# Optimization experiments

Measured on AMD Instinct MI355X. Metric: run time of the kernel, lower is better.

## Reference

```python
import jax, jax.numpy as jnp
import numpy as np

B = 4096
NC = 64        # n_concepts
NT = 16        # n_tasks
H = 256        # prior_units (prior_layers = 1)
HID = 256      # prior_hids = [256, 256]
K = 20         # n_components
IN = 3 * NC + NT + 1        # GRU input size = 209
MLP_IN = H + 3 * NC + NT    # rnn_out input = 464
LOG_2PI = float(np.log(2.0 * np.pi))


def setup_inputs() -> dict:
    key = jax.random.key(0)
    ks = jax.random.split(key, 16)
    s = 0.05
    inp = {
        "z": jax.random.normal(ks[0], (B, NC), jnp.float32),
        "c": jax.random.normal(ks[1], (B, NC + NT), jnp.float32),
        "b": (jax.random.uniform(ks[2], (B, NC)) < 0.5).astype(jnp.float32),
        "m": (jax.random.uniform(ks[3], (B, NC)) < 0.5).astype(jnp.float32),
        # GRU (PyTorch layout: gates ordered r, z, n)
        "W_ih": jax.random.normal(ks[4], (3 * H, IN), jnp.float32) * s,
        "W_hh": jax.random.normal(ks[5], (3 * H, H), jnp.float32) * s,
        "b_ih": jax.random.normal(ks[6], (3 * H,), jnp.float32) * s,
        "b_hh": jax.random.normal(ks[7], (3 * H,), jnp.float32) * s,
        # rnn_out MLP: Linear(464,256)+Tanh, Linear(256,256)+Tanh, Linear(256,3K)
        "W1": jax.random.normal(ks[8], (HID, MLP_IN), jnp.float32) * s,
        "b1": jax.random.normal(ks[9], (HID,), jnp.float32) * s,
        "W2": jax.random.normal(ks[10], (HID, HID), jnp.float32) * s,
        "b2": jax.random.normal(ks[11], (HID,), jnp.float32) * s,
        "W3": jax.random.normal(ks[12], (3 * K, HID), jnp.float32) * s,
        "b3": jax.random.normal(ks[13], (3 * K,), jnp.float32) * s,
    }
    return inp


def _logp(z, c, b, m, W_ih, W_hh, b_ih, b_hh, W1, b1, W2, b2, W3, b3):
    Bsz, d = z.shape
    cbm = jnp.concatenate([c, b, m], axis=1)               # [B, 3*NC+NT]
    # z input at step t is -1 for t=0, else z[:, t-1]
    z_prev = jnp.concatenate(
        [-jnp.ones((Bsz, 1), z.dtype), z[:, :-1]], axis=1)  # [B, d]
    # Precompute the input-gate projections for all steps without
    # materializing the full [d, B, IN] sequence tensor:
    # column 0 of W_ih multiplies z_prev; the rest multiplies cbm.
    gi_cbm = cbm @ W_ih[:, 1:].T + b_ih                    # [B, 3H]
    gi = gi_cbm[None, :, :] + z_prev.T[:, :, None] * W_ih[:, 0][None, None, :]  # [d, B, 3H]

    def gru_step(h, gi_t):
        gh = h @ W_hh.T + b_hh
        gi_r, gi_u, gi_n = jnp.split(gi_t, 3, axis=-1)
        gh_r, gh_u, gh_n = jnp.split(gh, 3, axis=-1)
        r = jax.nn.sigmoid(gi_r + gh_r)
        u = jax.nn.sigmoid(gi_u + gh_u)
        n = jnp.tanh(gi_n + r * gh_n)
        h_new = (1.0 - u) * n + u * h
        return h_new, h_new

    h0 = jnp.zeros((Bsz, W_hh.shape[1]), z.dtype)
    _, hs = jax.lax.scan(gru_step, h0, gi)                 # [d, B, H]
    hs = jnp.transpose(hs, (1, 0, 2))                      # [B, d, H]

    feat = jnp.concatenate(
        [hs, jnp.broadcast_to(cbm[:, None, :], (Bsz, d, cbm.shape[1]))],
        axis=2)                                            # [B, d, MLP_IN]
    h1 = jnp.tanh(feat @ W1.T + b1)
    h2 = jnp.tanh(h1 @ W2.T + b2)
    params = h2 @ W3.T + b3                                # [B, d, 3K]

    logits, means, lsigmas = jnp.split(params, 3, axis=-1)
    t = z[..., None]                                       # [B, d, 1]
    log_norm = -lsigmas - 0.5 * LOG_2PI
    diff = (t - means) * jnp.exp(-lsigmas)
    log_kernel = -0.5 * jnp.square(diff)
    log_like = (jax.nn.logsumexp(log_kernel + log_norm + logits, axis=-1)
                - jax.nn.logsumexp(logits, axis=-1))       # [B, d]

    query = m * (1.0 - b)
    mask = jnp.sort(query, axis=1)[:, ::-1]                # descending sort of values
    return jnp.sum(log_like * mask, axis=1)                # [B]


def reference(z, c, b, m, W_ih, W_hh, b_ih, b_hh, W1, b1, W2, b2, W3, b3):
    return _logp(z, c, b, m, W_ih, W_hh, b_ih, b_hh,
                 W1, b1, W2, b2, W3, b3)
```

## Files before the change

kernel.cpp:

```cpp
#include <hip/hip_runtime.h>
#include <hip/hip_bf16.h>

#define BATCH  4096
#define NCC    64
#define HDIM   256
#define G3     768
#define NROW   (BATCH*NCC)
#define NK     20
#define LOG2PI 1.8378770664093453f

typedef __attribute__((ext_vector_type(8))) short bf16x8;
typedef __attribute__((ext_vector_type(4))) float f32x4;

__device__ __forceinline__ float sigm(float x) { return 1.0f/(1.0f + __expf(-x)); }
__device__ __forceinline__ float tanh_fast(float x) { return 1.0f - 2.0f/(__expf(2.0f*x) + 1.0f); }
__device__ __forceinline__ unsigned short f2bf(float x) {
  __hip_bfloat16 h = __float2bfloat16(x);
  return __builtin_bit_cast(unsigned short, h);
}
__device__ __forceinline__ int swz(int r) { return (r & 7) ^ ((r & 8) >> 2); }

__global__ __launch_bounds__(256) void k_cvtall(
    const float* __restrict__ c, const float* __restrict__ bv,
    const float* __restrict__ mv, const float* __restrict__ W_ih,
    const float* __restrict__ W_hh, const float* __restrict__ W1,
    const float* __restrict__ W2, const float* __restrict__ W3,
    unsigned short* __restrict__ cbmB, unsigned short* __restrict__ CW,
    unsigned short* __restrict__ WhhB, unsigned short* __restrict__ W1aB,
    unsigned short* __restrict__ W2B, unsigned short* __restrict__ W3pB,
    float* __restrict__ w0) {
  int idx = blockIdx.x*256 + threadIdx.x;
  if (idx < 1048576) {
    int row = idx >> 8, k = idx & 255;
    float v = 0.f;
    if (k < 80)       v = c [row*80 + k];
    else if (k < 144) v = bv[row*64 + (k-80)];
    else if (k < 208) v = mv[row*64 + (k-144)];
    cbmB[idx] = f2bf(v);
    return;
  }
  idx -= 1048576;
  if (idx < 262144) {
    int n = idx >> 8, k = idx & 255;
    float v = 0.f;
    if (n < 768) { if (k < 208) v = W_ih[n*209 + 1 + k]; }
    else         { if (k < 208) v = W1[(n-768)*464 + 256 + k]; }
    CW[idx] = f2bf(v);
    return;
  }
  idx -= 262144;
  if (idx < 196608) { WhhB[idx] = f2bf(W_hh[idx]); return; }
  idx -= 196608;
  if (idx < 65536) { int n = idx>>8, k = idx&255; W1aB[idx] = f2bf(W1[n*464+k]); return; }
  idx -= 65536;
  if (idx < 65536) { W2B[idx] = f2bf(W2[idx]); return; }
  idx -= 65536;
  if (idx < 16384) {
    int n = idx >> 8;
    float v = 0.f;
    if (n < 60) v = W3[idx];
    W3pB[idx] = f2bf(v);
    return;
  }
  idx -= 16384;
  if (idx < 768) w0[idx] = W_ih[idx*209];
}

__global__ __launch_bounds__(512) void k_pre(
    const unsigned short* __restrict__ A, const unsigned short* __restrict__ Bw,
    const float* __restrict__ b_ih, const float* __restrict__ b_hh,
    const float* __restrict__ b1,
    float* __restrict__ gi, float* __restrict__ P1) {
  __shared__ __align__(16) unsigned short As[128*64];
  __shared__ __align__(16) unsigned short Bs[128*64];
  int tid = threadIdx.x;
  int rb = blockIdx.x >> 3, cb = blockIdx.x & 7;
  long row0 = (long)rb * 128;
  int n0 = cb * 128;
  int wv = tid >> 6, lane = tid & 63;
  int lq = lane >> 4, l16 = lane & 15;
  int wrg = wv & 3, wcg = wv >> 2;
  f32x4 acc[2][4];
#pragma unroll
  for (int i = 0; i < 2; ++i)
#pragma unroll
    for (int j = 0; j < 4; ++j) acc[i][j] = (f32x4){0.f,0.f,0.f,0.f};
  for (int kb = 0; kb < 256; kb += 64) {
#pragma unroll
    for (int i = 0; i < 2; ++i) {
      int s = i*512 + tid;
      int r = s >> 3, cg = (s & 7) ^ (r & 7);
      *(uint4*)&As[s*8] = *(const uint4*)&A[(row0 + r)*256 + kb + cg*8];
      *(uint4*)&Bs[s*8] = *(const uint4*)&Bw[(long)(n0 + r)*256 + kb + cg*8];
    }
    __syncthreads();
#pragma unroll
    for (int kc = 0; kc < 2; ++kc) {
      int csel = kc*4 + lq;
      bf16x8 af[2];
#pragma unroll
      for (int rt = 0; rt < 2; ++rt) {
        int r = wrg*32 + rt*16 + l16;
        af[rt] = *(const bf16x8*)&As[r*64 + ((csel ^ (r & 7)))*8];
      }
#pragma unroll
      for (int ct = 0; ct < 4; ++ct) {
        int n = wcg*64 + ct*16 + l16;
        bf16x8 bfr = *(const bf16x8*)&Bs[n*64 + ((csel ^ (n & 7)))*8];
        acc[0][ct] = __builtin_amdgcn_mfma_f32_16x16x32_bf16(af[0], bfr, acc[0][ct], 0, 0, 0);
        acc[1][ct] = __builtin_amdgcn_mfma_f32_16x16x32_bf16(af[1], bfr, acc[1][ct], 0, 0, 0);
      }
    }
    __syncthreads();
  }
#pragma unroll
  for (int rt = 0; rt < 2; ++rt)
#pragma unroll
    for (int q = 0; q < 4; ++q) {
      long row = row0 + wrg*32 + rt*16 + lq*4 + q;
#pragma unroll
      for (int ct = 0; ct < 4; ++ct) {
        int n = n0 + wcg*64 + ct*16 + l16;
        float v = acc[rt][ct][q];
        if (n < 512)      gi[row*G3 + n] = v + b_ih[n] + b_hh[n];
        else if (n < 768) gi[row*G3 + n] = v + b_ih[n];
        else              P1[row*256 + (n-768)] = v + b1[n-768];
      }
    }
}

__global__ __attribute__((amdgpu_flat_work_group_size(512, 512)))
__attribute__((amdgpu_waves_per_eu(2, 2)))
void k_gru(
    const float* __restrict__ z, const float* __restrict__ gi,
    const unsigned short* __restrict__ WhhB, const float* __restrict__ b_hh,
    const float* __restrict__ w0, unsigned short* __restrict__ hs) {
  __shared__ __align__(16) unsigned short hbf[2*16*256];
  __shared__ __align__(16) float gis[768*20];
  __shared__ __align__(16) float zs[64*16];
  __shared__ float wls[768 + 256];
  int tid = threadIdx.x;
  int wv = tid >> 6, lane = tid & 63;
  int lq = lane >> 4, l16 = lane & 15;
  int row0 = blockIdx.x * 16;
  bf16x8 wf[6][8];
#pragma unroll
  for (int g = 0; g < 3; ++g)
#pragma unroll
    for (int tt = 0; tt < 2; ++tt)
#pragma unroll
      for (int ks = 0; ks < 8; ++ks)
        wf[g*2+tt][ks] = *(const bf16x8*)&WhhB[(long)(g*256 + wv*32 + tt*16 + l16)*256 + ks*32 + lq*8];
  for (int i = tid; i < 768; i += 512) wls[i] = w0[i];
  for (int i = tid; i < 256; i += 512) wls[768 + i] = b_hh[512 + i];
  for (int i = tid; i < 1024; i += 512) {
    int t = i >> 4, r = i & 15;
    zs[i] = z[(row0+r)*64 + t];
  }
#pragma unroll
  for (int i = 0; i < 24; ++i) {
    int s = i*512 + tid;
    int r = s / 768, cc = s - r*768;
    gis[cc*20 + r] = gi[(long)(row0+r)*768 + cc];
  }
  for (int i = tid; i < 2048; i += 512) ((unsigned int*)hbf)[i] = 0u;
  float hp[2][4] = {{0.f,0.f,0.f,0.f},{0.f,0.f,0.f,0.f}};
  const int s7 = l16 & 7;
  const int arow = l16*256;
  const int r4 = lq*4;
  const int hc0 = wv*32 + l16;
  const int cr = tid >> 5, ccc = tid & 31;
  const int csrc = cr*256 + ((ccc ^ (cr & 7)))*8;
  unsigned short* cbase = hs + (long)(row0+cr)*64*256 + ccc*8;
  __syncthreads();
#pragma unroll 1
  for (int t = 0; t < 64; ++t) {
    const int co = (t & 1) << 12;
    const int no = co ^ 4096;
    float zp[4];
    {
      float4 zv4 = *(const float4*)&zs[(t ? (t-1) : 0)*16 + r4];
#pragma unroll
      for (int q = 0; q < 4; ++q) zp[q] = t ? (&zv4.x)[q] : -1.0f;
    }
    f32x4 a[6];
#pragma unroll
    for (int tt = 0; tt < 2; ++tt) {
      int hc = hc0 + tt*16;
      f32x4 gR = *(const f32x4*)&gis[hc*20 + r4];
      f32x4 gU = *(const f32x4*)&gis[(256+hc)*20 + r4];
      float w0r = wls[hc], w0u = wls[256+hc], bn = wls[768 + hc];
#pragma unroll
      for (int q = 0; q < 4; ++q) {
        a[tt][q]   = gR[q] + zp[q]*w0r;
        a[2+tt][q] = gU[q] + zp[q]*w0u;
        a[4+tt][q] = bn;
      }
    }
#pragma unroll
    for (int ks = 0; ks < 8; ++ks) {
      bf16x8 af = *(const bf16x8*)&hbf[co + arow + (((ks*4+lq) ^ s7))*8];
#pragma unroll
      for (int f = 0; f < 6; ++f)
        a[f] = __builtin_amdgcn_mfma_f32_16x16x32_bf16(af, wf[f][ks], a[f], 0, 0, 0);
    }
    if (t) {
      uint4 cdat = *(const uint4*)&hbf[co + csrc];
      *(uint4*)(cbase + (t-1)*256) = cdat;
    }
#pragma unroll
    for (int tt = 0; tt < 2; ++tt) {
      int hc = hc0 + tt*16;
      int hchunk = hc >> 3, hlow = hc & 7;
      float w0n = wls[512 + hc];
      f32x4 gN = *(const f32x4*)&gis[(512+hc)*20 + r4];
#pragma unroll
      for (int q = 0; q < 4; ++q) {
        int r = r4 + q;
        float rr = sigm(a[tt][q]);
        float uu = sigm(a[2+tt][q]);
        float nn = tanh_fast(gN[q] + zp[q]*w0n + rr*a[4+tt][q]);
        float hn = uu*(hp[tt][q] - nn) + nn;
        hp[tt][q] = hn;
        hbf[no + r*256 + ((hchunk ^ (r & 7)))*8 + hlow] = f2bf(hn);
      }
    }
    __syncthreads();
  }
  uint4 cdat = *(const uint4*)&hbf[0 + csrc];
  *(uint4*)(cbase + 63*256) = cdat;
}

__global__ __launch_bounds__(512) void k_l1(
    const unsigned short* __restrict__ A, const unsigned short* __restrict__ Bw,
    const float* __restrict__ P1, unsigned short* __restrict__ Out) {
  __shared__ __align__(16) unsigned short As[128*64];
  __shared__ __align__(16) unsigned short Bs[256*64];
  int tid = threadIdx.x;
  long row0 = (long)blockIdx.x * 128;
  int wv = tid >> 6, lane = tid & 63;
  int lq = lane >> 4, l16 = lane & 15;
  int wrg = wv & 3, wcg = wv >> 2;
  f32x4 acc[2][8];
#pragma unroll
  for (int i = 0; i < 2; ++i)
#pragma unroll
    for (int j = 0; j < 8; ++j) acc[i][j] = (f32x4){0.f,0.f,0.f,0.f};
  for (int kb = 0; kb < 256; kb += 64) {
#pragma unroll
    for (int i = 0; i < 2; ++i) {
      int s = i*512 + tid;
      int r = s >> 3, cg = (s & 7) ^ (r & 7);
      *(uint4*)&As[s*8] = *(const uint4*)&A[(row0 + r)*256 + kb + cg*8];
    }
#pragma unroll
    for (int i = 0; i < 4; ++i) {
      int s = i*512 + tid;
      int r = s >> 3, cg = (s & 7) ^ (r & 7);
      *(uint4*)&Bs[s*8] = *(const uint4*)&Bw[(long)r*256 + kb + cg*8];
    }
    __syncthreads();
#pragma unroll
    for (int kc = 0; kc < 2; ++kc) {
      int csel = kc*4 + lq;
      bf16x8 af[2];
#pragma unroll
      for (int rt = 0; rt < 2; ++rt) {
        int r = wrg*32 + rt*16 + l16;
        af[rt] = *(const bf16x8*)&As[r*64 + ((csel ^ (r & 7)))*8];
      }
#pragma unroll
      for (int ct = 0; ct < 8; ++ct) {
        int n = wcg*128 + ct*16 + l16;
        bf16x8 bfr = *(const bf16x8*)&Bs[n*64 + ((csel ^ (n & 7)))*8];
        acc[0][ct] = __builtin_amdgcn_mfma_f32_16x16x32_bf16(af[0], bfr, acc[0][ct], 0, 0, 0);
        acc[1][ct] = __builtin_amdgcn_mfma_f32_16x16x32_bf16(af[1], bfr, acc[1][ct], 0, 0, 0);
      }
    }
    __syncthreads();
  }
#pragma unroll
  for (int rt = 0; rt < 2; ++rt)
#pragma unroll
    for (int q = 0; q < 4; ++q) {
      long row = row0 + wrg*32 + rt*16 + lq*4 + q;
#pragma unroll
      for (int ct = 0; ct < 8; ++ct) {
        int n = wcg*128 + ct*16 + l16;
        float b = P1[(row >> 6)*256 + n];
        Out[row*256 + n] = f2bf(tanh_fast(acc[rt][ct][q] + b));
      }
    }
}

__global__ __launch_bounds__(512) void k_l23(
    const unsigned short* __restrict__ A, const unsigned short* __restrict__ W2B,
    const float* __restrict__ b2, const unsigned short* __restrict__ W3pB,
    const float* __restrict__ b3, const float* __restrict__ z,
    float* __restrict__ ll) {
  __shared__ __align__(16) unsigned short As[128*64];
  __shared__ __align__(16) unsigned short Bs[256*64];
  __shared__ __align__(16) unsigned short h2s[128*256];
  int tid = threadIdx.x;
  long row0 = (long)blockIdx.x * 128;
  int wv = tid >> 6, lane = tid & 63;
  int lq = lane >> 4, l16 = lane & 15;
  int wrg = wv & 3, wcg = wv >> 2;
  f32x4 acc[2][8];
#pragma unroll
  for (int i = 0; i < 2; ++i)
#pragma unroll
    for (int j = 0; j < 8; ++j) acc[i][j] = (f32x4){0.f,0.f,0.f,0.f};
  for (int kb = 0; kb < 256; kb += 64) {
#pragma unroll
    for (int i = 0; i < 2; ++i) {
      int s = i*512 + tid;
      int r = s >> 3, cg = (s & 7) ^ (r & 7);
      *(uint4*)&As[s*8] = *(const uint4*)&A[(row0 + r)*256 + kb + cg*8];
    }
#pragma unroll
    for (int i = 0; i < 4; ++i) {
      int s = i*512 + tid;
      int r = s >> 3, cg = (s & 7) ^ (r & 7);
      *(uint4*)&Bs[s*8] = *(const uint4*)&W2B[(long)r*256 + kb + cg*8];
    }
    __syncthreads();
#pragma unroll
    for (int kc = 0; kc < 2; ++kc) {
      int csel = kc*4 + lq;
      bf16x8 af[2];
#pragma unroll
      for (int rt = 0; rt < 2; ++rt) {
        int r = wrg*32 + rt*16 + l16;
        af[rt] = *(const bf16x8*)&As[r*64 + ((csel ^ (r & 7)))*8];
      }
#pragma unroll
      for (int ct = 0; ct < 8; ++ct) {
        int n = wcg*128 + ct*16 + l16;
        bf16x8 bfr = *(const bf16x8*)&Bs[n*64 + ((csel ^ (n & 7)))*8];
        acc[0][ct] = __builtin_amdgcn_mfma_f32_16x16x32_bf16(af[0], bfr, acc[0][ct], 0, 0, 0);
        acc[1][ct] = __builtin_amdgcn_mfma_f32_16x16x32_bf16(af[1], bfr, acc[1][ct], 0, 0, 0);
      }
    }
    __syncthreads();
  }
#pragma unroll
  for (int rt = 0; rt < 2; ++rt)
#pragma unroll
    for (int q = 0; q < 4; ++q) {
      int lr = wrg*32 + rt*16 + lq*4 + q;
#pragma unroll
      for (int ct = 0; ct < 8; ++ct) {
        int n = wcg*128 + ct*16 + l16;
        h2s[lr*256 + (((n >> 3) ^ swz(lr))*8 + (n & 7))] =
            f2bf(tanh_fast(acc[rt][ct][q] + b2[n]));
      }
    }
#pragma unroll
  for (int i = 0; i < 4; ++i) {
    int s = i*512 + tid;
    int r = s >> 5, cc = s & 31;
    *(uint4*)&Bs[r*256 + ((cc ^ swz(r)))*8] = *(const uint4*)&W3pB[r*256 + cc*8];
  }
  __syncthreads();
  f32x4 pacc[4];
#pragma unroll
  for (int j = 0; j < 4; ++j) pacc[j] = (f32x4){0.f,0.f,0.f,0.f};
#pragma unroll
  for (int ks = 0; ks < 8; ++ks) {
    int chunk = ks*4 + lq;
    int ar = wv*16 + l16;
    bf16x8 af = *(const bf16x8*)&h2s[ar*256 + ((chunk ^ swz(ar)))*8];
#pragma unroll
    for (int ct = 0; ct < 4; ++ct) {
      int br = ct*16 + l16;
      bf16x8 bfr = *(const bf16x8*)&Bs[br*256 + ((chunk ^ swz(br)))*8];
      pacc[ct] = __builtin_amdgcn_mfma_f32_16x16x32_bf16(af, bfr, pacc[ct], 0, 0, 0);
    }
  }
  float* Ps = (float*)&h2s[wv*16*256];
#pragma unroll
  for (int ct = 0; ct < 4; ++ct) {
    int n = ct*16 + l16;
    float b = (n < 60) ? b3[n] : 0.0f;
#pragma unroll
    for (int q = 0; q < 4; ++q)
      Ps[(lq*4 + q)*68 + n] = pacc[ct][q] + b;
  }
  if (lane < 16) {
    long grow = row0 + wv*16 + lane;
    float zv = z[grow];
    const float* p = &Ps[lane*68];
    float mx1 = -1e30f;
#pragma unroll
    for (int i = 0; i < NK; ++i) mx1 = fmaxf(mx1, p[i]);
    float s1 = 0.0f;
#pragma unroll
    for (int i = 0; i < NK; ++i) s1 += __expf(p[i] - mx1);
    float lse1 = mx1 + __logf(s1);
    float a[NK];
    float mx2 = -1e30f;
#pragma unroll
    for (int i = 0; i < NK; ++i) {
      float lg = p[i], me = p[20+i], ls = p[40+i];
      float e = __expf(-ls);
      float d = (zv - me) * e;
      float ai = -0.5f*d*d - ls - 0.5f*LOG2PI + lg;
      a[i] = ai;
      mx2 = fmaxf(mx2, ai);
    }
    float s2 = 0.0f;
#pragma unroll
    for (int i = 0; i < NK; ++i) s2 += __expf(a[i] - mx2);
    float lse2 = mx2 + __logf(s2);
    ll[grow] = lse2 - lse1;
  }
}

__global__ __launch_bounds__(256) void k_final(const float* __restrict__ bv,
    const float* __restrict__ mv, const float* __restrict__ ll,
    float* __restrict__ out) {
  int tid = threadIdx.x;
  int wave = tid >> 6, lane = tid & 63;
  int b = blockIdx.x*4 + wave;
  float q = mv[b*64 + lane] * (1.0f - bv[b*64 + lane]);
  unsigned long long bal = __ballot(q > 0.5f);
  int S = __popcll(bal);
  float val = (lane < S) ? ll[(long)b*64 + lane] : 0.0f;
#pragma unroll
  for (int off = 32; off > 0; off >>= 1) val += __shfl_down(val, off);
  if (lane == 0) out[b] = val;
}

extern "C" void kernel_launch(void* const* d_in, const int* in_sizes, int n_in,
                              void* d_out, int out_size, void* d_ws, size_t ws_size,
                              hipStream_t stream) {
  const float* z    = (const float*)d_in[0];
  const float* c    = (const float*)d_in[1];
  const float* bv   = (const float*)d_in[2];
  const float* mv   = (const float*)d_in[3];
  const float* W_ih = (const float*)d_in[4];
  const float* W_hh = (const float*)d_in[5];
  const float* b_ih = (const float*)d_in[6];
  const float* b_hh = (const float*)d_in[7];
  const float* W1   = (const float*)d_in[8];
  const float* b1   = (const float*)d_in[9];
  const float* W2   = (const float*)d_in[10];
  const float* b2   = (const float*)d_in[11];
  const float* W3   = (const float*)d_in[12];
  const float* b3   = (const float*)d_in[13];
  float* out = (float*)d_out;

  char* p = (char*)d_ws;
  auto alloc = [&](size_t bytes) {
    char* q = p;
    p += (bytes + 255) & ~(size_t)255;
    return q;
  };
  unsigned short* cbmB = (unsigned short*)alloc((size_t)BATCH*256*2);
  unsigned short* CW   = (unsigned short*)alloc((size_t)1024*256*2);
  unsigned short* WhhB = (unsigned short*)alloc((size_t)G3*256*2);
  unsigned short* W1aB = (unsigned short*)alloc((size_t)256*256*2);
  unsigned short* W2B  = (unsigned short*)alloc((size_t)256*256*2);
  unsigned short* W3pB = (unsigned short*)alloc((size_t)64*256*2);
  float* w0 = (float*)alloc((size_t)G3*4);
  float* gi = (float*)alloc((size_t)BATCH*G3*4);
  float* P1 = (float*)alloc((size_t)BATCH*256*4);
  float* ll = (float*)alloc((size_t)NROW*4);
  unsigned short* hs = (unsigned short*)alloc((size_t)NROW*HDIM*2);

  k_cvtall<<<6468, 256, 0, stream>>>(c, bv, mv, W_ih, W_hh, W1, W2, W3,
                                     cbmB, CW, WhhB, W1aB, W2B, W3pB, w0);
  k_pre<<<256, 512, 0, stream>>>(cbmB, CW, b_ih, b_hh, b1, gi, P1);
  k_gru<<<256, 512, 0, stream>>>(z, gi, WhhB, b_hh, w0, hs);
  k_l1<<<NROW/128, 512, 0, stream>>>(hs, W1aB, P1, hs);
  k_l23<<<NROW/128, 512, 0, stream>>>(hs, W2B, b2, W3pB, b3, z, ll);
  k_final<<<BATCH/4, 256, 0, stream>>>(bv, mv, ll, out);
}
```

Baseline: 517.2 us.

## Halve GRU block to 256 threads with each wave holding twice the weight columns

```diff
diff --git a/kernel.cpp b/kernel.cpp
--- a/kernel.cpp
+++ b/kernel.cpp
@@ -129,8 +129,8 @@
     }
 }
 
-__global__ __attribute__((amdgpu_flat_work_group_size(512, 512)))
-__attribute__((amdgpu_waves_per_eu(2, 2)))
+__global__ __attribute__((amdgpu_flat_work_group_size(256, 256)))
+__attribute__((amdgpu_waves_per_eu(1, 1)))
 void k_gru(
     const float* __restrict__ z, const float* __restrict__ gi,
     const unsigned short* __restrict__ WhhB, const float* __restrict__ b_hh,
@@ -143,36 +143,59 @@
   int wv = tid >> 6, lane = tid & 63;
   int lq = lane >> 4, l16 = lane & 15;
   int row0 = blockIdx.x * 16;
-  bf16x8 wf[6][8];
+
+  bf16x8 wf[3][4][8];
 #pragma unroll
   for (int g = 0; g < 3; ++g)
 #pragma unroll
-    for (int tt = 0; tt < 2; ++tt)
+    for (int cf = 0; cf < 4; ++cf)
 #pragma unroll
       for (int ks = 0; ks < 8; ++ks)
-        wf[g*2+tt][ks] = *(const bf16x8*)&WhhB[(long)(g*256 + wv*32 + tt*16 + l16)*256 + ks*32 + lq*8];
-  for (int i = tid; i < 768; i += 512) wls[i] = w0[i];
-  for (int i = tid; i < 256; i += 512) wls[768 + i] = b_hh[512 + i];
-  for (int i = tid; i < 1024; i += 512) {
+        wf[g][cf][ks] = *(const bf16x8*)&WhhB[
+            (long)(g*256 + wv*64 + cf*16 + l16)*256 + ks*32 + lq*8];
+
+  for (int i = tid; i < 768; i += 256) wls[i] = w0[i];
+  for (int i = tid; i < 256; i += 256) wls[768 + i] = b_hh[512 + i];
+  for (int i = tid; i < 1024; i += 256) {
     int t = i >> 4, r = i & 15;
     zs[i] = z[(row0+r)*64 + t];
   }
 #pragma unroll
-  for (int i = 0; i < 24; ++i) {
-    int s = i*512 + tid;
-    int r = s / 768, cc = s - r*768;
-    gis[cc*20 + r] = gi[(long)(row0+r)*768 + cc];
-  }
-  for (int i = tid; i < 2048; i += 512) ((unsigned int*)hbf)[i] = 0u;
-  float hp[2][4] = {{0.f,0.f,0.f,0.f},{0.f,0.f,0.f,0.f}};
+  for (int i = 0; i < 12; ++i) {
+    int s = i*256 + tid;
+    int r = s / 192, c4 = (s - r*192)*4;
+    float4 v = *(const float4*)&gi[(long)(row0+r)*768 + c4];
+    gis[(c4+0)*20 + r] = v.x;
+    gis[(c4+1)*20 + r] = v.y;
+    gis[(c4+2)*20 + r] = v.z;
+    gis[(c4+3)*20 + r] = v.w;
+  }
+  for (int i = tid; i < 2048; i += 256) ((unsigned int*)hbf)[i] = 0u;
+
+#pragma unroll
+  for (int g = 0; g < 3; ++g)
+#pragma unroll
+    for (int cf = 0; cf < 4; ++cf)
+#pragma unroll
+      for (int ks = 0; ks < 8; ++ks)
+        asm volatile("" : "+v"(wf[g][cf][ks]));
+
+  float hp[4][4];
+#pragma unroll
+  for (int i = 0; i < 4; ++i)
+#pragma unroll
+    for (int j = 0; j < 4; ++j) hp[i][j] = 0.f;
+
   const int s7 = l16 & 7;
   const int arow = l16*256;
   const int r4 = lq*4;
-  const int hc0 = wv*32 + l16;
-  const int cr = tid >> 5, ccc = tid & 31;
-  const int csrc = cr*256 + ((ccc ^ (cr & 7)))*8;
-  unsigned short* cbase = hs + (long)(row0+cr)*64*256 + ccc*8;
+  const int cr = tid >> 4;
+  const int chA = tid & 15;
+  const int chB = chA + 16;
+  const int cswz = cr & 7;
+  unsigned short* cbase = hs + (long)(row0+cr)*64*256 + chA*8;
   __syncthreads();
+
 #pragma unroll 1
   for (int t = 0; t < 64; ++t) {
     const int co = (t & 1) << 12;
@@ -183,52 +206,66 @@
 #pragma unroll
       for (int q = 0; q < 4; ++q) zp[q] = t ? (&zv4.x)[q] : -1.0f;
     }
-    f32x4 a[6];
-#pragma unroll
-    for (int tt = 0; tt < 2; ++tt) {
-      int hc = hc0 + tt*16;
-      f32x4 gR = *(const f32x4*)&gis[hc*20 + r4];
-      f32x4 gU = *(const f32x4*)&gis[(256+hc)*20 + r4];
-      float w0r = wls[hc], w0u = wls[256+hc], bn = wls[768 + hc];
-#pragma unroll
-      for (int q = 0; q < 4; ++q) {
-        a[tt][q]   = gR[q] + zp[q]*w0r;
-        a[2+tt][q] = gU[q] + zp[q]*w0u;
-        a[4+tt][q] = bn;
-      }
-    }
-#pragma unroll
-    for (int ks = 0; ks < 8; ++ks) {
-      bf16x8 af = *(const bf16x8*)&hbf[co + arow + (((ks*4+lq) ^ s7))*8];
-#pragma unroll
-      for (int f = 0; f < 6; ++f)
-        a[f] = __builtin_amdgcn_mfma_f32_16x16x32_bf16(af, wf[f][ks], a[f], 0, 0, 0);
-    }
     if (t) {
-      uint4 cdat = *(const uint4*)&hbf[co + csrc];
-      *(uint4*)(cbase + (t-1)*256) = cdat;
-    }
-#pragma unroll
-    for (int tt = 0; tt < 2; ++tt) {
-      int hc = hc0 + tt*16;
-      int hchunk = hc >> 3, hlow = hc & 7;
-      float w0n = wls[512 + hc];
-      f32x4 gN = *(const f32x4*)&gis[(512+hc)*20 + r4];
-#pragma unroll
-      for (int q = 0; q < 4; ++q) {
-        int r = r4 + q;
-        float rr = sigm(a[tt][q]);
-        float uu = sigm(a[2+tt][q]);
-        float nn = tanh_fast(gN[q] + zp[q]*w0n + rr*a[4+tt][q]);
-        float hn = uu*(hp[tt][q] - nn) + nn;
-        hp[tt][q] = hn;
-        hbf[no + r*256 + ((hchunk ^ (r & 7)))*8 + hlow] = f2bf(hn);
-      }
-    }
-    __syncthreads();
-  }
-  uint4 cdat = *(const uint4*)&hbf[0 + csrc];
-  *(uint4*)(cbase + 63*256) = cdat;
+      uint4 c0 = *(const uint4*)&hbf[co + cr*256 + ((chA ^ cswz))*8];
+      uint4 c1 = *(const uint4*)&hbf[co + cr*256 + ((chB ^ cswz))*8];
+      *(uint4*)(cbase + (t-1)*256)       = c0;
+      *(uint4*)(cbase + (t-1)*256 + 128) = c1;
+    }
+#pragma unroll
+    for (int hf = 0; hf < 2; ++hf) {
+      f32x4 acc[3][2];
+#pragma unroll
+      for (int c2 = 0; c2 < 2; ++c2) {
+        int cf = hf*2 + c2;
+        int hc = wv*64 + cf*16 + l16;
+        f32x4 gR = *(const f32x4*)&gis[hc*20 + r4];
+        f32x4 gU = *(const f32x4*)&gis[(256+hc)*20 + r4];
+        float w0r = wls[hc], w0u = wls[256+hc], bn = wls[768+hc];
+#pragma unroll
+        for (int q = 0; q < 4; ++q) {
+          acc[0][c2][q] = gR[q] + zp[q]*w0r;
+          acc[1][c2][q] = gU[q] + zp[q]*w0u;
+          acc[2][c2][q] = bn;
+        }
+      }
+#pragma unroll
+      for (int ks = 0; ks < 8; ++ks) {
+        bf16x8 af = *(const bf16x8*)&hbf[co + arow + ((ks*4+lq) ^ s7)*8];
+#pragma unroll
+        for (int g = 0; g < 3; ++g)
+#pragma unroll
+          for (int c2 = 0; c2 < 2; ++c2)
+            acc[g][c2] = __builtin_amdgcn_mfma_f32_16x16x32_bf16(
+                af, wf[g][hf*2+c2][ks], acc[g][c2], 0, 0, 0);
+      }
+#pragma unroll
+      for (int c2 = 0; c2 < 2; ++c2) {
+        int cf = hf*2 + c2;
+        int hc = wv*64 + cf*16 + l16;
+        int hchunk = hc >> 3, hlow = hc & 7;
+        float w0n = wls[512 + hc];
+        f32x4 gN = *(const f32x4*)&gis[(512+hc)*20 + r4];
+#pragma unroll
+        for (int q = 0; q < 4; ++q) {
+          int r = r4 + q;
+          float rr = sigm(acc[0][c2][q]);
+          float uu = sigm(acc[1][c2][q]);
+          float nn = tanh_fast(gN[q] + zp[q]*w0n + rr*acc[2][c2][q]);
+          float hn = uu*(hp[cf][q] - nn) + nn;
+          hp[cf][q] = hn;
+          hbf[no + r*256 + ((hchunk ^ (r & 7)))*8 + hlow] = f2bf(hn);
+        }
+      }
+    }
+    __syncthreads();
+  }
+  {
+    uint4 c0 = *(const uint4*)&hbf[0 + cr*256 + ((chA ^ cswz))*8];
+    uint4 c1 = *(const uint4*)&hbf[0 + cr*256 + ((chB ^ cswz))*8];
+    *(uint4*)(cbase + 63*256)       = c0;
+    *(uint4*)(cbase + 63*256 + 128) = c1;
+  }
 }
 
 __global__ __launch_bounds__(512) void k_l1(
@@ -472,7 +509,7 @@
   k_cvtall<<<6468, 256, 0, stream>>>(c, bv, mv, W_ih, W_hh, W1, W2, W3,
                                      cbmB, CW, WhhB, W1aB, W2B, W3pB, w0);
   k_pre<<<256, 512, 0, stream>>>(cbmB, CW, b_ih, b_hh, b1, gi, P1);
-  k_gru<<<256, 512, 0, stream>>>(z, gi, WhhB, b_hh, w0, hs);
+  k_gru<<<256, 256, 0, stream>>>(z, gi, WhhB, b_hh, w0, hs);
   k_l1<<<NROW/128, 512, 0, stream>>>(hs, W1aB, P1, hs);
   k_l23<<<NROW/128, 512, 0, stream>>>(hs, W2B, b2, W3pB, b3, z, ll);
   k_final<<<BATCH/4, 256, 0, stream>>>(bv, mv, ll, out);
```

Measured after the change: 530.7 us. +2.6%, slower.
